# Performance work log

Hardware: AMD Instinct MI355X
Metric: run time of the kernel (lower is better)

## Reference

```python
import jax, jax.numpy as jnp
import numpy as np

HIDDEN = 1024
HEADS = 16
HEAD_DIM = HIDDEN // HEADS


def setup_inputs() -> dict:
    key = jax.random.key(0)
    ks = jax.random.split(key, 4)
    B, S, H = 2, 2048, HIDDEN
    scale = 1.0 / np.sqrt(H)
    return {
        "inputs": jax.random.normal(ks[0], (B, S, H), dtype=jnp.float32),
        "mask": jnp.ones((B, S), dtype=jnp.int32),
        "Wq": jax.random.normal(ks[1], (H, H), dtype=jnp.float32) * scale,
        "bq": jnp.zeros((H,), dtype=jnp.float32),
        "Wk": jax.random.normal(ks[2], (H, H), dtype=jnp.float32) * scale,
        "bk": jnp.zeros((H,), dtype=jnp.float32),
        "Wv": jax.random.normal(ks[3], (H, H), dtype=jnp.float32) * scale,
        "bv": jnp.zeros((H,), dtype=jnp.float32),
    }


def _split_heads(x, B, S):
    # [B,S,H] -> [B,heads,S,head_dim]
    return x.reshape(B, S, HEADS, HEAD_DIM).transpose(0, 2, 1, 3)


def reference(inputs, mask, Wq, bq, Wk, bk, Wv, bv):
    B, S, H = inputs.shape
    q = _split_heads(inputs @ Wq.T + bq, B, S)
    k = _split_heads(inputs @ Wk.T + bk, B, S)
    v = _split_heads(inputs @ Wv.T + bv, B, S)
    scores = jnp.einsum("bhqd,bhkd->bhqk", q, k) / jnp.sqrt(
        jnp.asarray(HEAD_DIM, dtype=inputs.dtype))
    # mask broadcast [B,1,1,S]; zeros -> -inf
    scores = jnp.where(mask[:, None, None, :] == 0, -jnp.inf, scores)
    attn = jax.nn.softmax(scores, axis=-1)
    context = jnp.einsum("bhqk,bhkd->bhqd", attn, v)
    return context.transpose(0, 2, 1, 3).reshape(B, S, H)
```

## Files before the change

kernel.cpp:

```cpp
#include <hip/hip_runtime.h>
#include <hip/hip_fp16.h>

constexpr int S_LEN  = 2048;
constexpr int HID    = 1024;
constexpr int HEADS  = 16;
constexpr int HDIM   = 64;
constexpr int BATCH  = 2;
constexpr int BH     = BATCH * HEADS;
constexpr int M_ROWS = BATCH * S_LEN;

typedef _Float16 half8  __attribute__((ext_vector_type(8)));
typedef _Float16 half4v __attribute__((ext_vector_type(4)));
typedef _Float16 half2v __attribute__((ext_vector_type(2)));
typedef float    f32x4  __attribute__((ext_vector_type(4)));
typedef float    f32x16 __attribute__((ext_vector_type(16)));
typedef unsigned uint4v __attribute__((ext_vector_type(4)));

constexpr float EXP2_OFF = -11.541560327111707f;
constexpr float Q_SCALE  = 0.18033688011112042f;

__global__ __launch_bounds__(256) void cvt_kernel(
    const float* __restrict__ X,  const float* __restrict__ Wq,
    const float* __restrict__ Wk, const float* __restrict__ Wv,
    const int* __restrict__ mask,
    _Float16* __restrict__ Xh,  _Float16* __restrict__ Wqh,
    _Float16* __restrict__ Wkh, _Float16* __restrict__ Wvh,
    float* __restrict__ maskF)
{
    const int blk = blockIdx.x;
    if (blk >= 3584) {
        const int loc = blk - 3584;
        const size_t e = ((size_t)loc * 256 + threadIdx.x) * 8;
        #pragma unroll
        for (int i = 0; i < 8; ++i)
            maskF[e + i] = mask[e + i] ? EXP2_OFF : -1.0e30f;
        return;
    }
    const float* src; _Float16* dst; int loc;
    if (blk < 2048)      { src = X;  dst = Xh;  loc = blk; }
    else if (blk < 2560) { src = Wq; dst = Wqh; loc = blk - 2048; }
    else if (blk < 3072) { src = Wk; dst = Wkh; loc = blk - 2560; }
    else                 { src = Wv; dst = Wvh; loc = blk - 3072; }
    const size_t e = ((size_t)loc * 256 + threadIdx.x) * 8;
    float4 a = *reinterpret_cast<const float4*>(&src[e]);
    float4 b = *reinterpret_cast<const float4*>(&src[e + 4]);
    half8 h = { (_Float16)a.x, (_Float16)a.y, (_Float16)a.z, (_Float16)a.w,
                (_Float16)b.x, (_Float16)b.y, (_Float16)b.z, (_Float16)b.w };
    *reinterpret_cast<half8*>(&dst[e]) = h;
}

__device__ __forceinline__ void async_cp16(_Float16* lds, const _Float16* g) {
    __builtin_amdgcn_global_load_lds(
        (const __attribute__((address_space(1))) void*)g,
        (__attribute__((address_space(3))) void*)lds, 16, 0, 0);
}
__device__ __forceinline__ void async_cp4(float* lds, const float* g) {
    __builtin_amdgcn_global_load_lds(
        (const __attribute__((address_space(1))) void*)g,
        (__attribute__((address_space(3))) void*)lds, 4, 0, 0);
}

__device__ __forceinline__ void permlane32_swap(unsigned &x, unsigned &y) {
    asm("v_permlane32_swap_b32 %0, %1" : "+v"(x), "+v"(y));
}

__global__ __launch_bounds__(256) void qkv_proj_kernel(
    const _Float16* __restrict__ Xh,
    const _Float16* __restrict__ Wqh, const _Float16* __restrict__ Wkh,
    const _Float16* __restrict__ Wvh,
    const float* __restrict__ bq, const float* __restrict__ bk,
    const float* __restrict__ bv,
    _Float16* __restrict__ Qo, _Float16* __restrict__ Ko,
    _Float16* __restrict__ Vt)
{
    const int mode = blockIdx.z;
    const _Float16* W    = (mode == 0) ? Wqh : (mode == 1) ? Wkh : Wvh;
    const float*    bias = (mode == 0) ? bq  : (mode == 1) ? bk  : bv;

    const int m0 = blockIdx.x * 128, n0 = blockIdx.y * 128;
    const int tid = threadIdx.x, wave = tid >> 6, lane = tid & 63;
    const int l31 = lane & 31, kg = lane >> 5;

    __shared__ _Float16 SMEM[24576];

    f32x16 acc[2][2];
    #pragma unroll
    for (int mt = 0; mt < 2; ++mt)
        #pragma unroll
        for (int nt = 0; nt < 2; ++nt)
            #pragma unroll
            for (int i = 0; i < 16; ++i) acc[mt][nt][i] = 0.f;

    const int wm = (wave & 1) * 64, wn = (wave >> 1) * 64;

    const int srow = tid >> 2, spos = tid & 3;
    auto stage = [&](int k0, int b) {
        _Float16* Asb = SMEM + b * 8192;
        _Float16* Bsb = Asb + 4096;
        #pragma unroll
        for (int j = 0; j < 2; ++j) {
            const int row = srow + j * 64;
            const int sch = spos ^ ((row + (row >> 2)) & 3);
            async_cp16(&Asb[j * 2048 + tid * 8],
                       &Xh[(size_t)(m0 + row) * HID + k0 + sch * 8]);
            async_cp16(&Bsb[j * 2048 + tid * 8],
                       &W [(size_t)(n0 + row) * HID + k0 + sch * 8]);
        }
    };

    constexpr int NIT = HID / 32;
    stage(0, 0);
    stage(32, 1);
    int buf = 0;

    for (int it = 0; it < NIT; ++it) {
        asm volatile("s_waitcnt vmcnt(4)" ::: "memory");
        __builtin_amdgcn_s_barrier();
        asm volatile("" ::: "memory");

        {
            int it2 = it + 2; if (it2 >= NIT) it2 -= NIT;
            int nb  = buf + 2; if (nb >= 3) nb -= 3;
            stage(it2 * 32, nb);
        }

        _Float16* Asb = SMEM + buf * 8192;
        _Float16* Bsb = Asb + 4096;

        #pragma unroll
        for (int c = 0; c < 2; ++c) {
            const int k8 = c * 2 + kg;
            half8 af[2], bf[2];
            #pragma unroll
            for (int mt = 0; mt < 2; ++mt) {
                const int row = wm + mt * 32 + l31;
                const int g   = (row + (row >> 2)) & 3;
                af[mt] = *reinterpret_cast<const half8*>(
                    &Asb[row * 32 + ((k8 ^ g) * 8)]);
            }
            #pragma unroll
            for (int nt = 0; nt < 2; ++nt) {
                const int row = wn + nt * 32 + l31;
                const int g   = (row + (row >> 2)) & 3;
                bf[nt] = *reinterpret_cast<const half8*>(
                    &Bsb[row * 32 + ((k8 ^ g) * 8)]);
            }
            __builtin_amdgcn_s_setprio(1);
            #pragma unroll
            for (int mt = 0; mt < 2; ++mt)
                #pragma unroll
                for (int nt = 0; nt < 2; ++nt)
                    acc[mt][nt] = __builtin_amdgcn_mfma_f32_32x32x16_f16(
                        af[mt], bf[nt], acc[mt][nt], 0, 0, 0);
            __builtin_amdgcn_s_setprio(0);
        }
        if (++buf == 3) buf = 0;
    }
    asm volatile("s_waitcnt vmcnt(0)" ::: "memory");
    __syncthreads();

    _Float16* T = SMEM + wave * 4608;

    const int nn  = n0 + wn;
    const int hh  = nn >> 6;
    const int mm  = m0 + wm;
    const int bb  = mm >> 11;
    const int bhv = bb * HEADS + hh;
    const int s0  = mm & 2047;
    const int rowg = lane >> 3, chunk = lane & 7;

    if (mode < 2) {
        _Float16* Out = (mode == 0) ? Qo : Ko;
        #pragma unroll
        for (int nt = 0; nt < 2; ++nt) {
            const int col = nt * 32 + l31;
            float bias_n = bias[nn + col];
            #pragma unroll
            for (int mt = 0; mt < 2; ++mt)
                #pragma unroll
                for (int r = 0; r < 16; ++r) {
                    const int row_l = (r & 3) + 8 * (r >> 2) + 4 * kg;
                    float v = acc[mt][nt][r] + bias_n;
                    if (mode == 0) v *= Q_SCALE;
                    T[(mt * 32 + row_l) * 72 + col] = (_Float16)v;
                }
        }
        asm volatile("s_waitcnt lgkmcnt(0)" ::: "memory");
        #pragma unroll
        for (int j = 0; j < 8; ++j) {
            const int sr = j * 8 + rowg;
            half8 v = *reinterpret_cast<const half8*>(&T[sr * 72 + chunk * 8]);
            *reinterpret_cast<half8*>(
                &Out[((size_t)bhv * S_LEN + s0 + sr) * HDIM + chunk * 8]) = v;
        }
    } else {
        #pragma unroll
        for (int nt = 0; nt < 2; ++nt) {
            const int col = nt * 32 + l31;
            const float bias_n = bias[nn + col];
            #pragma unroll
            for (int mt = 0; mt < 2; ++mt)
                #pragma unroll
                for (int rg = 0; rg < 4; ++rg) {
                    half4v t = { (_Float16)(acc[mt][nt][rg * 4 + 0] + bias_n),
                                 (_Float16)(acc[mt][nt][rg * 4 + 1] + bias_n),
                                 (_Float16)(acc[mt][nt][rg * 4 + 2] + bias_n),
                                 (_Float16)(acc[mt][nt][rg * 4 + 3] + bias_n) };
                    const int s_off = mt * 32 + 8 * rg + 4 * kg;
                    *reinterpret_cast<half4v*>(&T[col * 72 + s_off]) = t;
                }
        }
        asm volatile("s_waitcnt lgkmcnt(0)" ::: "memory");
        #pragma unroll
        for (int j = 0; j < 8; ++j) {
            const int dr = j * 8 + rowg;
            half8 v = *reinterpret_cast<const half8*>(&T[dr * 72 + chunk * 8]);
            *reinterpret_cast<half8*>(
                &Vt[((size_t)bhv * HDIM + dr) * S_LEN + s0 + chunk * 8]) = v;
        }
    }
}

__global__ __launch_bounds__(512, 4) void attn_kernel(
    const _Float16* __restrict__ Q, const _Float16* __restrict__ K,
    const _Float16* __restrict__ Vt, const float* __restrict__ maskF,
    float* __restrict__ Out)
{
    const int id   = blockIdx.x;
    const int xcd  = id & 7;
    const int bh   = xcd * 4 + ((id >> 3) & 3);
    const int qt   = id >> 5;
    const int b = bh >> 4, h = bh & 15;
    const int tid = threadIdx.x, wave = tid >> 6, lane = tid & 63;
    const int l31 = lane & 31, kg = lane >> 5;
    const int wq = wave & 3, wk = wave >> 2;

    __shared__ _Float16 SMEM[3 * 8192];
    __shared__ float    Ms[3][8][64];

    const _Float16* Qb = Q  + (size_t)bh * S_LEN * HDIM;
    const _Float16* Kb = K  + (size_t)bh * S_LEN * HDIM;
    const _Float16* Vb = Vt + (size_t)bh * HDIM * S_LEN;
    const float*    mb = maskF + b * S_LEN;

    const int qrow = qt * 128 + wq * 32 + l31;

    half8 qf[4];
    #pragma unroll
    for (int kc = 0; kc < 4; ++kc)
        qf[kc] = *reinterpret_cast<const half8*>(
            &Qb[(size_t)qrow * HDIM + kc * 16 + kg * 8]);
    asm volatile("s_waitcnt vmcnt(0)" ::: "memory");

    f32x16 acc[2];
    #pragma unroll
    for (int dt = 0; dt < 2; ++dt)
        #pragma unroll
        for (int i = 0; i < 16; ++i) acc[dt][i] = 0.f;
    float den = 0.f;

    const int srow = tid >> 3;
    const int slot = tid & 7;
    auto stage = [&](int tile, int bufsel) {
        const int kb   = tile * 64;
        const int csrc = slot ^ (srow & 7);
        _Float16* Kd = SMEM + bufsel * 8192;
        async_cp16(&Kd[tid * 8], &Kb[(size_t)(kb + srow) * HDIM + csrc * 8]);
        async_cp16(&Kd[4096 + tid * 8],
                   &Vb[(size_t)srow * S_LEN + kb + csrc * 8]);
        async_cp4(&Ms[bufsel][wave][lane], &mb[kb + lane]);
    };

    constexpr int NT = S_LEN / 64;
    stage(0, 0);
    stage(1, 1);
    int buf = 0;
    const int rsw = l31 & 7;

    for (int t = 0; t < NT; ++t) {
        asm volatile("s_waitcnt vmcnt(3)" ::: "memory");
        __builtin_amdgcn_s_barrier();
        asm volatile("" ::: "memory");

        {
            int nt2 = t + 2; if (nt2 >= NT) nt2 -= NT;
            int nb  = buf + 2; if (nb >= 3) nb -= 3;
            stage(nt2, nb);
        }

        const _Float16* Kl = SMEM + buf * 8192;
        const _Float16* Vl = Kl + 4096;
        const float*    Mw = Ms[buf][wave];

        float4 mm0 = *reinterpret_cast<const float4*>(&Mw[wk * 32 + 0 + kg * 4]);
        float4 mm1 = *reinterpret_cast<const float4*>(&Mw[wk * 32 + 8 + kg * 4]);
        float4 mm2 = *reinterpret_cast<const float4*>(&Mw[wk * 32 + 16 + kg * 4]);
        float4 mm3 = *reinterpret_cast<const float4*>(&Mw[wk * 32 + 24 + kg * 4]);
        f32x16 sc = { mm0.x, mm0.y, mm0.z, mm0.w,
                      mm1.x, mm1.y, mm1.z, mm1.w,
                      mm2.x, mm2.y, mm2.z, mm2.w,
                      mm3.x, mm3.y, mm3.z, mm3.w };

        const _Float16* Krow = &Kl[(wk * 32 + l31) * 64];
        half8 kf[4];
        #pragma unroll
        for (int kc = 0; kc < 4; ++kc)
            kf[kc] = *reinterpret_cast<const half8*>(
                &Krow[((kc * 2 + kg) ^ rsw) * 8]);
        __builtin_amdgcn_s_setprio(1);
        #pragma unroll
        for (int kc = 0; kc < 4; ++kc)
            sc = __builtin_amdgcn_mfma_f32_32x32x16_f16(kf[kc], qf[kc], sc, 0, 0, 0);
        __builtin_amdgcn_s_setprio(0);

        half8 vf[2][2];
        #pragma unroll
        for (int dt = 0; dt < 2; ++dt) {
            const _Float16* Vrow = &Vl[(dt * 32 + l31) * 64];
            #pragma unroll
            for (int hh = 0; hh < 2; ++hh)
                vf[dt][hh] = *reinterpret_cast<const half8*>(
                    &Vrow[((wk * 4 + hh * 2 + kg) ^ rsw) * 8]);
        }

        float p[16];
        #pragma unroll
        for (int r = 0; r < 16; ++r)
            p[r] = __builtin_amdgcn_exp2f(sc[r]);
        den += (((p[0] + p[1]) + (p[2] + p[3])) +
                ((p[4] + p[5]) + (p[6] + p[7]))) +
               (((p[8] + p[9]) + (p[10] + p[11])) +
                ((p[12] + p[13]) + (p[14] + p[15])));

        #pragma unroll
        for (int hh = 0; hh < 2; ++hh) {
            unsigned a0 = __builtin_bit_cast(unsigned,
                __builtin_amdgcn_cvt_pkrtz(p[hh * 8 + 0], p[hh * 8 + 1]));
            unsigned a1 = __builtin_bit_cast(unsigned,
                __builtin_amdgcn_cvt_pkrtz(p[hh * 8 + 2], p[hh * 8 + 3]));
            unsigned b0 = __builtin_bit_cast(unsigned,
                __builtin_amdgcn_cvt_pkrtz(p[hh * 8 + 4], p[hh * 8 + 5]));
            unsigned b1 = __builtin_bit_cast(unsigned,
                __builtin_amdgcn_cvt_pkrtz(p[hh * 8 + 6], p[hh * 8 + 7]));
            permlane32_swap(a0, b0);
            permlane32_swap(a1, b1);
            uint4v pd = { a0, a1, b0, b1 };
            half8 pf = __builtin_bit_cast(half8, pd);
            __builtin_amdgcn_s_setprio(1);
            acc[0] = __builtin_amdgcn_mfma_f32_32x32x16_f16(
                vf[0][hh], pf, acc[0], 0, 0, 0);
            acc[1] = __builtin_amdgcn_mfma_f32_32x32x16_f16(
                vf[1][hh], pf, acc[1], 0, 0, 0);
            __builtin_amdgcn_s_setprio(0);
        }
        if (++buf == 3) buf = 0;
    }

    asm volatile("s_waitcnt vmcnt(0)" ::: "memory");
    __syncthreads();

    den += __shfl_xor(den, 32, 64);

    float* LF = reinterpret_cast<float*>(SMEM);
    float* DF = reinterpret_cast<float*>(Ms);
    if (wk == 1) {
        float* wbase = LF + (wq * 64 + lane) * 36;
        #pragma unroll
        for (int dt = 0; dt < 2; ++dt)
            #pragma unroll
            for (int g = 0; g < 4; ++g) {
                float4 o = { acc[dt][g * 4 + 0], acc[dt][g * 4 + 1],
                             acc[dt][g * 4 + 2], acc[dt][g * 4 + 3] };
                *reinterpret_cast<float4*>(&wbase[dt * 16 + g * 4]) = o;
            }
        if (kg == 0) DF[wq * 32 + l31] = den;
    }
    __syncthreads();
    if (wk == 0) {
        const float* rbase = LF + (wq * 64 + lane) * 36;
        const float inv = 1.0f / (den + DF[wq * 32 + l31]);
        float* orow = Out + ((size_t)(b * S_LEN + qrow)) * HID + h * HDIM;
        #pragma unroll
        for (int dt = 0; dt < 2; ++dt)
            #pragma unroll
            for (int g = 0; g < 4; ++g) {
                float4 pv = *reinterpret_cast<const float4*>(
                    &rbase[dt * 16 + g * 4]);
                float4 o = { (acc[dt][g * 4 + 0] + pv.x) * inv,
                             (acc[dt][g * 4 + 1] + pv.y) * inv,
                             (acc[dt][g * 4 + 2] + pv.z) * inv,
                             (acc[dt][g * 4 + 3] + pv.w) * inv };
                *reinterpret_cast<float4*>(&orow[dt * 32 + g * 8 + kg * 4]) = o;
            }
    }
}

extern "C" void kernel_launch(void* const* d_in, const int* in_sizes, int n_in,
                              void* d_out, int out_size, void* d_ws, size_t ws_size,
                              hipStream_t stream) {
    const float* X  = (const float*)d_in[0];
    const int*   mk = (const int*)  d_in[1];
    const float* Wq = (const float*)d_in[2];
    const float* bq = (const float*)d_in[3];
    const float* Wk = (const float*)d_in[4];
    const float* bk = (const float*)d_in[5];
    const float* Wv = (const float*)d_in[6];
    const float* bv = (const float*)d_in[7];
    float* out = (float*)d_out;

    _Float16* Xh  = (_Float16*)d_ws;
    _Float16* Wqh = Xh  + (size_t)M_ROWS * HID;
    _Float16* Wkh = Wqh + (size_t)HID * HID;
    _Float16* Wvh = Wkh + (size_t)HID * HID;
    _Float16* Q   = Wvh + (size_t)HID * HID;
    _Float16* K   = Q   + (size_t)BH * S_LEN * HDIM;
    _Float16* Vt  = K   + (size_t)BH * S_LEN * HDIM;
    float*    maskF = (float*)(Vt + (size_t)BH * S_LEN * HDIM);

    cvt_kernel<<<3586, 256, 0, stream>>>(X, Wq, Wk, Wv, mk, Xh, Wqh, Wkh, Wvh, maskF);

    dim3 gp(M_ROWS / 128, HID / 128, 3);
    qkv_proj_kernel<<<gp, 256, 0, stream>>>(Xh, Wqh, Wkh, Wvh, bq, bk, bv, Q, K, Vt);

    attn_kernel<<<512, 512, 0, stream>>>(Q, K, Vt, maskF, out);
}
```

Before: 167.3 us.

## Split QKV projection tile across 8 waves with 32x64 per-wave subtiles

The QKV projection block goes from 256 to 512 threads, so each of the 8 waves computes a 32x64 subtile instead of a 64x64 one. Each thread now stages one 16-byte chunk per operand instead of two, the vmcnt wait is adjusted to match, and the epilogue transpose buffers shrink. This halves accumulator registers per wave and adds waves per CU to hide latency. In exchange, A-fragment reuse per wave drops and B fragments are reloaded by twice as many waves, which adds LDS traffic.

```diff
diff --git a/kernel.cpp b/kernel.cpp
--- a/kernel.cpp
+++ b/kernel.cpp
@@ -64,7 +64,7 @@
     asm("v_permlane32_swap_b32 %0, %1" : "+v"(x), "+v"(y));
 }
 
-__global__ __launch_bounds__(256) void qkv_proj_kernel(
+__global__ __launch_bounds__(512, 6) void qkv_proj_kernel(
     const _Float16* __restrict__ Xh,
     const _Float16* __restrict__ Wqh, const _Float16* __restrict__ Wkh,
     const _Float16* __restrict__ Wvh,
@@ -83,29 +83,24 @@
 
     __shared__ _Float16 SMEM[24576];
 
-    f32x16 acc[2][2];
+    const int wm = (wave & 3) * 32;
+    const int wn = (wave >> 2) * 64;
+
+    f32x16 acc[2];
     #pragma unroll
-    for (int mt = 0; mt < 2; ++mt)
-        #pragma unroll
-        for (int nt = 0; nt < 2; ++nt)
-            #pragma unroll
-            for (int i = 0; i < 16; ++i) acc[mt][nt][i] = 0.f;
-
-    const int wm = (wave & 1) * 64, wn = (wave >> 1) * 64;
+    for (int nt = 0; nt < 2; ++nt)
+        #pragma unroll
+        for (int i = 0; i < 16; ++i) acc[nt][i] = 0.f;
 
     const int srow = tid >> 2, spos = tid & 3;
     auto stage = [&](int k0, int b) {
         _Float16* Asb = SMEM + b * 8192;
         _Float16* Bsb = Asb + 4096;
-        #pragma unroll
-        for (int j = 0; j < 2; ++j) {
-            const int row = srow + j * 64;
-            const int sch = spos ^ ((row + (row >> 2)) & 3);
-            async_cp16(&Asb[j * 2048 + tid * 8],
-                       &Xh[(size_t)(m0 + row) * HID + k0 + sch * 8]);
-            async_cp16(&Bsb[j * 2048 + tid * 8],
-                       &W [(size_t)(n0 + row) * HID + k0 + sch * 8]);
-        }
+        const int sch = spos ^ ((srow + (srow >> 2)) & 3);
+        async_cp16(&Asb[tid * 8],
+                   &Xh[(size_t)(m0 + srow) * HID + k0 + sch * 8]);
+        async_cp16(&Bsb[tid * 8],
+                   &W [(size_t)(n0 + srow) * HID + k0 + sch * 8]);
     };
 
     constexpr int NIT = HID / 32;
@@ -113,8 +108,11 @@
     stage(32, 1);
     int buf = 0;
 
+    const int arow = wm + l31;
+    const int ag   = (arow + (arow >> 2)) & 3;
+
     for (int it = 0; it < NIT; ++it) {
-        asm volatile("s_waitcnt vmcnt(4)" ::: "memory");
+        asm volatile("s_waitcnt vmcnt(2)" ::: "memory");
         __builtin_amdgcn_s_barrier();
         asm volatile("" ::: "memory");
 
@@ -130,14 +128,9 @@
         #pragma unroll
         for (int c = 0; c < 2; ++c) {
             const int k8 = c * 2 + kg;
-            half8 af[2], bf[2];
-            #pragma unroll
-            for (int mt = 0; mt < 2; ++mt) {
-                const int row = wm + mt * 32 + l31;
-                const int g   = (row + (row >> 2)) & 3;
-                af[mt] = *reinterpret_cast<const half8*>(
-                    &Asb[row * 32 + ((k8 ^ g) * 8)]);
-            }
+            half8 af = *reinterpret_cast<const half8*>(
+                &Asb[arow * 32 + ((k8 ^ ag) * 8)]);
+            half8 bf[2];
             #pragma unroll
             for (int nt = 0; nt < 2; ++nt) {
                 const int row = wn + nt * 32 + l31;
@@ -147,11 +140,9 @@
             }
             __builtin_amdgcn_s_setprio(1);
             #pragma unroll
-            for (int mt = 0; mt < 2; ++mt)
-                #pragma unroll
-                for (int nt = 0; nt < 2; ++nt)
-                    acc[mt][nt] = __builtin_amdgcn_mfma_f32_32x32x16_f16(
-                        af[mt], bf[nt], acc[mt][nt], 0, 0, 0);
+            for (int nt = 0; nt < 2; ++nt)
+                acc[nt] = __builtin_amdgcn_mfma_f32_32x32x16_f16(
+                    af, bf[nt], acc[nt], 0, 0, 0);
             __builtin_amdgcn_s_setprio(0);
         }
         if (++buf == 3) buf = 0;
@@ -159,7 +150,7 @@
     asm volatile("s_waitcnt vmcnt(0)" ::: "memory");
     __syncthreads();
 
-    _Float16* T = SMEM + wave * 4608;
+    _Float16* T = SMEM + wave * 2560;
 
     const int nn  = n0 + wn;
     const int hh  = nn >> 6;
@@ -167,7 +158,6 @@
     const int bb  = mm >> 11;
     const int bhv = bb * HEADS + hh;
     const int s0  = mm & 2047;
-    const int rowg = lane >> 3, chunk = lane & 7;
 
     if (mode < 2) {
         _Float16* Out = (mode == 0) ? Qo : Ko;
@@ -176,18 +166,17 @@
             const int col = nt * 32 + l31;
             float bias_n = bias[nn + col];
             #pragma unroll
-            for (int mt = 0; mt < 2; ++mt)
-                #pragma unroll
-                for (int r = 0; r < 16; ++r) {
-                    const int row_l = (r & 3) + 8 * (r >> 2) + 4 * kg;
-                    float v = acc[mt][nt][r] + bias_n;
-                    if (mode == 0) v *= Q_SCALE;
-                    T[(mt * 32 + row_l) * 72 + col] = (_Float16)v;
-                }
+            for (int r = 0; r < 16; ++r) {
+                const int row_l = (r & 3) + 8 * (r >> 2) + 4 * kg;
+                float v = acc[nt][r] + bias_n;
+                if (mode == 0) v *= Q_SCALE;
+                T[row_l * 72 + col] = (_Float16)v;
+            }
         }
         asm volatile("s_waitcnt lgkmcnt(0)" ::: "memory");
-        #pragma unroll
-        for (int j = 0; j < 8; ++j) {
+        const int rowg = lane >> 3, chunk = lane & 7;
+        #pragma unroll
+        for (int j = 0; j < 4; ++j) {
             const int sr = j * 8 + rowg;
             half8 v = *reinterpret_cast<const half8*>(&T[sr * 72 + chunk * 8]);
             *reinterpret_cast<half8*>(
@@ -199,22 +188,21 @@
             const int col = nt * 32 + l31;
             const float bias_n = bias[nn + col];
             #pragma unroll
-            for (int mt = 0; mt < 2; ++mt)
-                #pragma unroll
-                for (int rg = 0; rg < 4; ++rg) {
-                    half4v t = { (_Float16)(acc[mt][nt][rg * 4 + 0] + bias_n),
-                                 (_Float16)(acc[mt][nt][rg * 4 + 1] + bias_n),
-                                 (_Float16)(acc[mt][nt][rg * 4 + 2] + bias_n),
-                                 (_Float16)(acc[mt][nt][rg * 4 + 3] + bias_n) };
-                    const int s_off = mt * 32 + 8 * rg + 4 * kg;
-                    *reinterpret_cast<half4v*>(&T[col * 72 + s_off]) = t;
-                }
+            for (int rg = 0; rg < 4; ++rg) {
+                half4v t = { (_Float16)(acc[nt][rg * 4 + 0] + bias_n),
+                             (_Float16)(acc[nt][rg * 4 + 1] + bias_n),
+                             (_Float16)(acc[nt][rg * 4 + 2] + bias_n),
+                             (_Float16)(acc[nt][rg * 4 + 3] + bias_n) };
+                const int s_off = 8 * rg + 4 * kg;
+                *reinterpret_cast<half4v*>(&T[col * 40 + s_off]) = t;
+            }
         }
         asm volatile("s_waitcnt lgkmcnt(0)" ::: "memory");
-        #pragma unroll
-        for (int j = 0; j < 8; ++j) {
-            const int dr = j * 8 + rowg;
-            half8 v = *reinterpret_cast<const half8*>(&T[dr * 72 + chunk * 8]);
+        const int chunk = lane & 3;
+        #pragma unroll
+        for (int j = 0; j < 4; ++j) {
+            const int dr = j * 16 + (lane >> 2);
+            half8 v = *reinterpret_cast<const half8*>(&T[dr * 40 + chunk * 8]);
             *reinterpret_cast<half8*>(
                 &Vt[((size_t)bhv * HDIM + dr) * S_LEN + s0 + chunk * 8]) = v;
         }
@@ -420,7 +408,7 @@
     cvt_kernel<<<3586, 256, 0, stream>>>(X, Wq, Wk, Wv, mk, Xh, Wqh, Wkh, Wvh, maskF);
 
     dim3 gp(M_ROWS / 128, HID / 128, 3);
-    qkv_proj_kernel<<<gp, 256, 0, stream>>>(Xh, Wqh, Wkh, Wvh, bq, bk, bv, Q, K, Vt);
+    qkv_proj_kernel<<<gp, 512, 0, stream>>>(Xh, Wqh, Wkh, Wvh, bq, bk, bv, Q, K, Vt);
 
     attn_kernel<<<512, 512, 0, stream>>>(Q, K, Vt, maskF, out);
 }
```

New measurement: 168.0 us. Within noise of the previous version (+0.5%).
